# Kernel optimization log

Hardware: AMD Instinct MI355X
Metric: run time of the kernel (lower is better)

Reference implementation:

```python
import jax, jax.numpy as jnp
import numpy as np

B, F_IN, C_NODES, M = 8, 32, 256, 64
C_OUT = 64
ORDER = 2
N_BASES = 3


def setup_inputs() -> dict:
    key = jax.random.key(0)
    ks = jax.random.split(key, 6)
    x = jax.random.normal(ks[0], (B, F_IN, C_NODES, M), dtype=jnp.float32)
    base0 = jax.random.uniform(ks[1], (B, M, C_NODES, C_NODES), dtype=jnp.float32) / C_NODES
    base1 = jax.random.uniform(ks[2], (B, M, C_NODES, C_NODES), dtype=jnp.float32) / C_NODES
    base2 = jax.random.uniform(ks[3], (B, M, C_NODES, C_NODES), dtype=jnp.float32) / C_NODES
    c_cat = (ORDER * N_BASES + 1) * F_IN  # 224
    W = jax.random.normal(ks[4], (C_OUT, c_cat), dtype=jnp.float32) * (1.0 / np.sqrt(c_cat))
    b = jnp.zeros((C_OUT,), dtype=jnp.float32)
    return {"x": x, "base0": base0, "base1": base1, "base2": base2, "W": W, "b": b}


def _nconv(x, A):
    # x: [B, F, n, M], A: [B, M, n, v] -> [B, F, v, M]
    return jnp.einsum('bfnm,bmnv->bfvm', x, A)


def reference(x, base0, base1, base2, W, b):
    out = [x]
    for A in (base0, base1, base2):
        x1 = _nconv(x, A)
        out.append(x1)
        for _ in range(2, ORDER + 1):
            x1 = _nconv(x1, A)
            out.append(x1)
    h = jnp.concatenate(out, axis=1)  # [B, 7F, C, M]
    # 1x1 conv == channel-mixing GEMM
    y = jnp.einsum('of,bfcm->bocm', W, h) + b[None, :, None, None]
    return y
```

## Files before the change

kernel.cpp:

```cpp
#include <hip/hip_runtime.h>

typedef __attribute__((ext_vector_type(8))) short short8;
typedef __attribute__((ext_vector_type(4))) float floatx4;
typedef unsigned short u16;
typedef unsigned int u32;

#define GETC(v, hw) ((hw)==0 ? (v).x : (hw)==1 ? (v).y : (hw)==2 ? (v).z : (v).w)
#define MFMA16(a,b,c) __builtin_amdgcn_mfma_f32_16x16x32_bf16((a),(b),(c),0,0,0)

__device__ __forceinline__ u16 f2bf(float f) {
  u32 u = __builtin_bit_cast(u32, f);
  u += 0x7fffu + ((u >> 16) & 1u);
  return (u16)(u >> 16);
}
__device__ __forceinline__ u32 pk2(float a, float b) {
  return (u32)f2bf(a) | ((u32)f2bf(b) << 16);
}

__global__ __launch_bounds__(256) void tk_f2b(const float* __restrict__ in,
                                              u16* __restrict__ out,
                                              int NI, int NJ) {
  __shared__ float tile[64][65];
  const int tid = threadIdx.x;
  const long long base = (long long)blockIdx.z * NI * NJ;
  const int i0 = blockIdx.x * 64, j0 = blockIdx.y * 64;
#pragma unroll
  for (int p = 0; p < 4; ++p) {
    int i = p * 16 + (tid >> 4);
    int jl = (tid & 15) * 4;
    float4 v = *(const float4*)(in + base + (long long)(i0 + i) * NJ + j0 + jl);
    tile[i][jl + 0] = v.x; tile[i][jl + 1] = v.y;
    tile[i][jl + 2] = v.z; tile[i][jl + 3] = v.w;
  }
  __syncthreads();
#pragma unroll
  for (int p = 0; p < 4; ++p) {
    int j = p * 16 + (tid >> 4);
    int il = (tid & 15) * 4;
    float e0 = tile[il + 0][j], e1 = tile[il + 1][j];
    float e2 = tile[il + 2][j], e3 = tile[il + 3][j];
    uint2 o; o.x = pk2(e0, e1); o.y = pk2(e2, e3);
    *(uint2*)(out + base + (long long)(j0 + j) * NI + i0 + il) = o;
  }
}

__global__ __launch_bounds__(256) void tk_f2f(const float* __restrict__ in,
                                              float* __restrict__ out,
                                              int NI, int NJ) {
  __shared__ float tile[64][65];
  const int tid = threadIdx.x;
  const long long base = (long long)blockIdx.z * NI * NJ;
  const int i0 = blockIdx.x * 64, j0 = blockIdx.y * 64;
#pragma unroll
  for (int p = 0; p < 4; ++p) {
    int i = p * 16 + (tid >> 4);
    int jl = (tid & 15) * 4;
    float4 v = *(const float4*)(in + base + (long long)(i0 + i) * NJ + j0 + jl);
    tile[i][jl + 0] = v.x; tile[i][jl + 1] = v.y;
    tile[i][jl + 2] = v.z; tile[i][jl + 3] = v.w;
  }
  __syncthreads();
#pragma unroll
  for (int p = 0; p < 4; ++p) {
    int j = p * 16 + (tid >> 4);
    int il = (tid & 15) * 4;
    float4 o;
    o.x = tile[il + 0][j]; o.y = tile[il + 1][j];
    o.z = tile[il + 2][j]; o.w = tile[il + 3][j];
    *(float4*)(out + base + (long long)(j0 + j) * NI + i0 + il) = o;
  }
}

__global__ __launch_bounds__(256, 1) void gcn_main(
    const u16* __restrict__ xT, const float* __restrict__ A0,
    const float* __restrict__ A1, const float* __restrict__ A2,
    const float* __restrict__ Wm, const float* __restrict__ bias,
    float* __restrict__ yT) {
  __shared__ __align__(16) unsigned char smem[163840];
  unsigned char* fragA  = smem;
  unsigned char* fragX1 = smem + 131072;
  unsigned char* fragH  = smem + 147456;

  const int tid  = threadIdx.x;
  const int w    = tid >> 6;
  const int lane = tid & 63;
  const int q    = lane >> 4;
  const int s    = lane & 15;
  const int wg   = blockIdx.x;

  const float* Ab0 = A0 + (size_t)wg * 65536;
  const float* Ab1 = A1 + (size_t)wg * 65536;
  const float* Ab2 = A2 + (size_t)wg * 65536;

  short8 xa[2][8];
  const u16* xp = xT + (size_t)wg * 8192;
#pragma unroll
  for (int mr = 0; mr < 2; ++mr)
#pragma unroll
    for (int k = 0; k < 8; ++k)
      xa[mr][k] = *(const short8*)(xp + (16 * mr + s) * 256 + 32 * k + 8 * q);

  const int bn = tid >> 5, bv = tid & 31;
  const int v0 = bv * 8;
  uint4 stg[4][8];
  auto loadStage = [&](const float* Ai) {
#pragma unroll
    for (int p = 0; p < 4; ++p) {
      int n0 = p * 64 + bn * 8;
#pragma unroll
      for (int jj = 0; jj < 8; ++jj) {
        const float* rp = Ai + (size_t)(n0 + jj) * 256 + v0;
        float4 lo = *(const float4*)rp;
        float4 hi = *(const float4*)(rp + 4);
        uint4 r;
        r.x = pk2(lo.x, lo.y); r.y = pk2(lo.z, lo.w);
        r.z = pk2(hi.x, hi.y); r.w = pk2(hi.z, hi.w);
        stg[p][jj] = r;
      }
    }
  };
  auto stageToLds = [&]() {
#pragma unroll
    for (int p = 0; p < 4; ++p) {
      int n0 = p * 64 + bn * 8;
      int kst = n0 >> 5, qst = (n0 >> 3) & 3;
#pragma unroll
      for (int i = 0; i < 8; ++i) {
        int v = v0 + i;
        int tg = v >> 4, sl = v & 15;
        u32 sel = (i & 1) ? 0x07060302u : 0x05040100u;
        const int hw = i >> 1;
        u32 d0 = __builtin_amdgcn_perm(GETC(stg[p][1], hw), GETC(stg[p][0], hw), sel);
        u32 d1 = __builtin_amdgcn_perm(GETC(stg[p][3], hw), GETC(stg[p][2], hw), sel);
        u32 d2 = __builtin_amdgcn_perm(GETC(stg[p][5], hw), GETC(stg[p][4], hw), sel);
        u32 d3 = __builtin_amdgcn_perm(GETC(stg[p][7], hw), GETC(stg[p][6], hw), sel);
        int phys = (qst * 16 + sl) ^ (tg & 7);
        uint4 val; val.x = d0; val.y = d1; val.z = d2; val.w = d3;
        *(uint4*)(fragA + (((kst * 16 + tg) * 64 + phys) << 4)) = val;
      }
    }
  };

  loadStage(Ab0);

#pragma unroll
  for (int mr = 0; mr < 2; ++mr)
#pragma unroll
    for (int kk = 0; kk < 8; ++kk) {
      if ((kk >> 1) != w) continue;
#pragma unroll
      for (int jj = 0; jj < 8; ++jj) {
        int c = 32 * kk + 8 * q + jj;
        int f = 16 * mr + s;
        int off = (((c >> 4) * 64 + (f >> 3) * 16 + (c & 15)) << 4) + 2 * (f & 7);
        *(u16*)(fragH + off) = (u16)xa[mr][kk][jj];
      }
    }

  floatx4 yacc[4][4];
#pragma unroll
  for (int mr = 0; mr < 4; ++mr)
#pragma unroll
    for (int t = 0; t < 4; ++t) yacc[mr][t] = (floatx4){0.f, 0.f, 0.f, 0.f};

  auto finalGemm = [&](int jblk) {
    short8 wf[4], hf[4];
#pragma unroll
    for (int mr = 0; mr < 4; ++mr) {
      const float* wp = Wm + (16 * mr + s) * 224 + 32 * jblk + 8 * q;
      float4 lo = *(const float4*)wp;
      float4 hi = *(const float4*)(wp + 4);
      union { uint4 u; short8 v; } r;
      r.u.x = pk2(lo.x, lo.y); r.u.y = pk2(lo.z, lo.w);
      r.u.z = pk2(hi.x, hi.y); r.u.w = pk2(hi.z, hi.w);
      wf[mr] = r.v;
    }
#pragma unroll
    for (int t = 0; t < 4; ++t)
      hf[t] = *(const short8*)(fragH + (((4 * w + t) * 64 + lane) << 4));
#pragma unroll
    for (int mr = 0; mr < 4; ++mr)
#pragma unroll
      for (int t = 0; t < 4; ++t)
        yacc[mr][t] = MFMA16(wf[mr], hf[t], yacc[mr][t]);
  };
  auto writeH = [&](const floatx4 (&acc)[2][4]) {
#pragma unroll
    for (int mr = 0; mr < 2; ++mr)
#pragma unroll
      for (int t = 0; t < 4; ++t)
#pragma unroll
        for (int r = 0; r < 4; ++r) {
          int F = 16 * mr + 4 * q + r;
          int off = (((4 * w + t) * 64 + (F >> 3) * 16 + s) << 4) + 2 * (F & 7);
          *(u16*)(fragH + off) = f2bf(acc[mr][t][r]);
        }
  };
  auto writeX1 = [&](const floatx4 (&acc)[2][4]) {
#pragma unroll
    for (int mr = 0; mr < 2; ++mr)
#pragma unroll
      for (int t = 0; t < 4; ++t) {
        int Cc = 64 * w + 16 * t + s;
        int kk = Cc >> 5, qq = (Cc >> 3) & 3, jj = Cc & 7;
#pragma unroll
        for (int r = 0; r < 4; ++r) {
          int off = (((mr * 8 + kk) * 64 + qq * 16 + 4 * q + r) << 4) + 2 * jj;
          *(u16*)(fragX1 + off) = f2bf(acc[mr][t][r]);
        }
      }
  };

  __syncthreads();
  finalGemm(0);

#pragma unroll 1
  for (int ib = 0; ib < 3; ++ib) {
    __syncthreads();
    stageToLds();
    if (ib < 2) loadStage(ib == 0 ? Ab1 : Ab2);
    __syncthreads();

    floatx4 h1[2][4];
#pragma unroll
    for (int mr = 0; mr < 2; ++mr)
#pragma unroll
      for (int t = 0; t < 4; ++t) h1[mr][t] = (floatx4){0.f, 0.f, 0.f, 0.f};
#pragma unroll
    for (int k = 0; k < 8; ++k) {
      short8 bf[4];
#pragma unroll
      for (int t = 0; t < 4; ++t) {
        int tg = 4 * w + t;
        bf[t] = *(const short8*)(fragA + (((k * 16 + tg) * 64 + (lane ^ (tg & 7))) << 4));
      }
#pragma unroll
      for (int mr = 0; mr < 2; ++mr)
#pragma unroll
        for (int t = 0; t < 4; ++t)
          h1[mr][t] = MFMA16(xa[mr][k], bf[t], h1[mr][t]);
    }
    writeX1(h1);
    writeH(h1);
    __syncthreads();
    finalGemm(1 + 2 * ib);

    floatx4 h2[2][4];
#pragma unroll
    for (int mr = 0; mr < 2; ++mr)
#pragma unroll
      for (int t = 0; t < 4; ++t) h2[mr][t] = (floatx4){0.f, 0.f, 0.f, 0.f};
#pragma unroll
    for (int k = 0; k < 8; ++k) {
      short8 a0 = *(const short8*)(fragX1 + ((k * 64 + lane) << 4));
      short8 a1 = *(const short8*)(fragX1 + (((8 + k) * 64 + lane) << 4));
      short8 bf[4];
#pragma unroll
      for (int t = 0; t < 4; ++t) {
        int tg = 4 * w + t;
        bf[t] = *(const short8*)(fragA + (((k * 16 + tg) * 64 + (lane ^ (tg & 7))) << 4));
      }
#pragma unroll
      for (int t = 0; t < 4; ++t) {
        h2[0][t] = MFMA16(a0, bf[t], h2[0][t]);
        h2[1][t] = MFMA16(a1, bf[t], h2[1][t]);
      }
    }
    __syncthreads();
    writeH(h2);
    __syncthreads();
    finalGemm(2 + 2 * ib);
  }

  float* yp = yT + (size_t)wg * 16384;
#pragma unroll
  for (int mr = 0; mr < 4; ++mr) {
    float br[4];
#pragma unroll
    for (int r = 0; r < 4; ++r) br[r] = bias[16 * mr + 4 * q + r];
#pragma unroll
    for (int t = 0; t < 4; ++t) {
      int c = 64 * w + 16 * t + s;
#pragma unroll
      for (int r = 0; r < 4; ++r) {
        int o = 16 * mr + 4 * q + r;
        yp[o * 256 + c] = yacc[mr][t][r] + br[r];
      }
    }
  }
}

extern "C" void kernel_launch(void* const* d_in, const int* in_sizes, int n_in,
                              void* d_out, int out_size, void* d_ws, size_t ws_size,
                              hipStream_t stream) {
  const float* x    = (const float*)d_in[0];
  const float* b0   = (const float*)d_in[1];
  const float* b1   = (const float*)d_in[2];
  const float* b2   = (const float*)d_in[3];
  const float* Wm   = (const float*)d_in[4];
  const float* bias = (const float*)d_in[5];
  u16*   xT  = (u16*)d_ws;
  float* yTs = (float*)((char*)d_ws + 8388608);
  float* out = (float*)d_out;

  tk_f2b<<<dim3(128, 1, 8), 256, 0, stream>>>(x, xT, 8192, 64);
  gcn_main<<<dim3(512), 256, 0, stream>>>(xT, b0, b1, b2, Wm, bias, yTs);
  tk_f2f<<<dim3(1, 256, 8), 256, 0, stream>>>(yTs, out, 64, 16384);
}
```

Measured before the change: 443.9 us.

## Stream A tiles via global_load_lds ring buffer, halve LDS for two blocks/CU

Replaces the register-staged full 128KB bf16 copy of each adjacency matrix in LDS with a 3-slot fp32 ring buffer filled by async global_load_lds. Each k-chunk is streamed and converted to bf16 at fragment-read time. The A matrix is re-streamed for both the order-1 and order-2 passes. This cuts LDS to 80KB so two workgroups can share a CU, and it overlaps global loads with MFMA, but the adjacency data is now read from global memory twice and converted repeatedly. It also drops several block barriers, relying on per-wave private ring slices plus vmcnt waits, which risks races around the fragH/fragX1 writes.

```diff
diff --git a/kernel.cpp b/kernel.cpp
--- a/kernel.cpp
+++ b/kernel.cpp
@@ -5,8 +5,26 @@
 typedef unsigned short u16;
 typedef unsigned int u32;
 
-#define GETC(v, hw) ((hw)==0 ? (v).x : (hw)==1 ? (v).y : (hw)==2 ? (v).z : (v).w)
 #define MFMA16(a,b,c) __builtin_amdgcn_mfma_f32_16x16x32_bf16((a),(b),(c),0,0,0)
+
+#define GLD_LDS16(src, dst)                                                    \
+  __builtin_amdgcn_global_load_lds(                                            \
+      (const __attribute__((address_space(1))) u32*)(const u32*)(src),         \
+      (__attribute__((address_space(3))) u32*)(u32*)(dst), 16, 0, 0)
+
+#define WAITVM(N)                                                              \
+  do {                                                                         \
+    asm volatile("s_waitcnt vmcnt(" #N ")" ::: "memory");                      \
+    __builtin_amdgcn_sched_barrier(0);                                         \
+  } while (0)
+
+#define WAITLGKM0() asm volatile("s_waitcnt lgkmcnt(0)" ::: "memory")
+
+__device__ __forceinline__ void bar_lds() {
+  WAITLGKM0();
+  __builtin_amdgcn_s_barrier();
+  asm volatile("" ::: "memory");
+}
 
 __device__ __forceinline__ u16 f2bf(float f) {
   u32 u = __builtin_bit_cast(u32, f);
@@ -71,15 +89,15 @@
   }
 }
 
-__global__ __launch_bounds__(256, 1) void gcn_main(
+__global__ __launch_bounds__(256, 2) void gcn_main(
     const u16* __restrict__ xT, const float* __restrict__ A0,
     const float* __restrict__ A1, const float* __restrict__ A2,
     const float* __restrict__ Wm, const float* __restrict__ bias,
     float* __restrict__ yT) {
-  __shared__ __align__(16) unsigned char smem[163840];
-  unsigned char* fragA  = smem;
-  unsigned char* fragX1 = smem + 131072;
-  unsigned char* fragH  = smem + 147456;
+  __shared__ __align__(16) unsigned char smem[81920];
+  unsigned char* ring   = smem;
+  unsigned char* fragX1 = smem + 49152;
+  unsigned char* fragH  = smem + 65536;
 
   const int tid  = threadIdx.x;
   const int w    = tid >> 6;
@@ -88,9 +106,26 @@
   const int s    = lane & 15;
   const int wg   = blockIdx.x;
 
-  const float* Ab0 = A0 + (size_t)wg * 65536;
-  const float* Ab1 = A1 + (size_t)wg * 65536;
-  const float* Ab2 = A2 + (size_t)wg * 65536;
+  const float* Acur  = A0 + (size_t)wg * 65536;
+  const float* Anxt  = A1 + (size_t)wg * 65536;
+  const float* Alast = A2 + (size_t)wg * 65536;
+
+  const int lrow = (lane >> 4) << 8;
+  const int lc0  = (w << 6) + ((lane & 15) << 2);
+  const int lc1  = lc0 ^ 16;
+  char* wring = (char*)ring + (w << 12);
+
+  auto stage = [&](const float* Ap, int c, int slot) {
+#pragma unroll
+    for (int i = 0; i < 4; ++i) {
+      const float* src = Ap + (c << 12) + (i << 10) + lrow + ((i & 2) ? lc1 : lc0);
+      GLD_LDS16(src, wring + slot * 16384 + (i << 10));
+    }
+  };
+
+  stage(Acur, 0, 0);
+  stage(Acur, 1, 1);
+  stage(Acur, 2, 2);
 
   short8 xa[2][8];
   const u16* xp = xT + (size_t)wg * 8192;
@@ -99,49 +134,6 @@
 #pragma unroll
     for (int k = 0; k < 8; ++k)
       xa[mr][k] = *(const short8*)(xp + (16 * mr + s) * 256 + 32 * k + 8 * q);
-
-  const int bn = tid >> 5, bv = tid & 31;
-  const int v0 = bv * 8;
-  uint4 stg[4][8];
-  auto loadStage = [&](const float* Ai) {
-#pragma unroll
-    for (int p = 0; p < 4; ++p) {
-      int n0 = p * 64 + bn * 8;
-#pragma unroll
-      for (int jj = 0; jj < 8; ++jj) {
-        const float* rp = Ai + (size_t)(n0 + jj) * 256 + v0;
-        float4 lo = *(const float4*)rp;
-        float4 hi = *(const float4*)(rp + 4);
-        uint4 r;
-        r.x = pk2(lo.x, lo.y); r.y = pk2(lo.z, lo.w);
-        r.z = pk2(hi.x, hi.y); r.w = pk2(hi.z, hi.w);
-        stg[p][jj] = r;
-      }
-    }
-  };
-  auto stageToLds = [&]() {
-#pragma unroll
-    for (int p = 0; p < 4; ++p) {
-      int n0 = p * 64 + bn * 8;
-      int kst = n0 >> 5, qst = (n0 >> 3) & 3;
-#pragma unroll
-      for (int i = 0; i < 8; ++i) {
-        int v = v0 + i;
-        int tg = v >> 4, sl = v & 15;
-        u32 sel = (i & 1) ? 0x07060302u : 0x05040100u;
-        const int hw = i >> 1;
-        u32 d0 = __builtin_amdgcn_perm(GETC(stg[p][1], hw), GETC(stg[p][0], hw), sel);
-        u32 d1 = __builtin_amdgcn_perm(GETC(stg[p][3], hw), GETC(stg[p][2], hw), sel);
-        u32 d2 = __builtin_amdgcn_perm(GETC(stg[p][5], hw), GETC(stg[p][4], hw), sel);
-        u32 d3 = __builtin_amdgcn_perm(GETC(stg[p][7], hw), GETC(stg[p][6], hw), sel);
-        int phys = (qst * 16 + sl) ^ (tg & 7);
-        uint4 val; val.x = d0; val.y = d1; val.z = d2; val.w = d3;
-        *(uint4*)(fragA + (((kst * 16 + tg) * 64 + phys) << 4)) = val;
-      }
-    }
-  };
-
-  loadStage(Ab0);
 
 #pragma unroll
   for (int mr = 0; mr < 2; ++mr)
@@ -211,38 +203,55 @@
       }
   };
 
-  __syncthreads();
+  auto fetchB = [&](int sl0, int sl1, short8 (&bf)[4]) {
+    const char* bse = (const char*)ring + ((q >= 2) ? sl1 : sl0) * 16384 +
+                      (w << 12) + ((q & 1) << 11);
+    const int pvx = (q & 1) << 4;
+#pragma unroll
+    for (int t = 0; t < 4; ++t) {
+      const float* fp = (const float*)(bse + ((((t << 4) + s) ^ pvx) << 2));
+      union { uint4 u; short8 v; } r;
+      r.u.x = pk2(fp[0],   fp[64]);
+      r.u.y = pk2(fp[128], fp[192]);
+      r.u.z = pk2(fp[256], fp[320]);
+      r.u.w = pk2(fp[384], fp[448]);
+      bf[t] = r.v;
+    }
+  };
+
   finalGemm(0);
 
 #pragma unroll 1
   for (int ib = 0; ib < 3; ++ib) {
-    __syncthreads();
-    stageToLds();
-    if (ib < 2) loadStage(ib == 0 ? Ab1 : Ab2);
-    __syncthreads();
-
     floatx4 h1[2][4];
 #pragma unroll
     for (int mr = 0; mr < 2; ++mr)
 #pragma unroll
       for (int t = 0; t < 4; ++t) h1[mr][t] = (floatx4){0.f, 0.f, 0.f, 0.f};
 #pragma unroll
-    for (int k = 0; k < 8; ++k) {
+    for (int kk = 0; kk < 8; ++kk) {
+      if (kk < 7) WAITVM(4); else WAITVM(0);
       short8 bf[4];
-#pragma unroll
-      for (int t = 0; t < 4; ++t) {
-        int tg = 4 * w + t;
-        bf[t] = *(const short8*)(fragA + (((k * 16 + tg) * 64 + (lane ^ (tg & 7))) << 4));
-      }
+      fetchB((2 * kk) % 3, (2 * kk + 1) % 3, bf);
 #pragma unroll
       for (int mr = 0; mr < 2; ++mr)
 #pragma unroll
         for (int t = 0; t < 4; ++t)
-          h1[mr][t] = MFMA16(xa[mr][k], bf[t], h1[mr][t]);
-    }
+          h1[mr][t] = MFMA16(xa[mr][kk], bf[t], h1[mr][t]);
+      WAITLGKM0();
+      if (kk < 6) {
+        stage(Acur, 2 * kk + 3, (2 * kk + 3) % 3);
+        stage(Acur, 2 * kk + 4, (2 * kk + 4) % 3);
+      } else if (kk == 6) {
+        stage(Acur, 15, 0);
+      } else {
+        stage(Acur, 0, 0); stage(Acur, 1, 1); stage(Acur, 2, 2);
+      }
+    }
+    bar_lds();
     writeX1(h1);
     writeH(h1);
-    __syncthreads();
+    bar_lds();
     finalGemm(1 + 2 * ib);
 
     floatx4 h2[2][4];
@@ -251,25 +260,31 @@
 #pragma unroll
       for (int t = 0; t < 4; ++t) h2[mr][t] = (floatx4){0.f, 0.f, 0.f, 0.f};
 #pragma unroll
-    for (int k = 0; k < 8; ++k) {
-      short8 a0 = *(const short8*)(fragX1 + ((k * 64 + lane) << 4));
-      short8 a1 = *(const short8*)(fragX1 + (((8 + k) * 64 + lane) << 4));
+    for (int kk = 0; kk < 8; ++kk) {
+      if (kk < 7) WAITVM(4); else WAITVM(0);
       short8 bf[4];
-#pragma unroll
-      for (int t = 0; t < 4; ++t) {
-        int tg = 4 * w + t;
-        bf[t] = *(const short8*)(fragA + (((k * 16 + tg) * 64 + (lane ^ (tg & 7))) << 4));
-      }
+      fetchB((2 * kk) % 3, (2 * kk + 1) % 3, bf);
+      short8 a0 = *(const short8*)(fragX1 + ((kk * 64 + lane) << 4));
+      short8 a1 = *(const short8*)(fragX1 + (((8 + kk) * 64 + lane) << 4));
 #pragma unroll
       for (int t = 0; t < 4; ++t) {
         h2[0][t] = MFMA16(a0, bf[t], h2[0][t]);
         h2[1][t] = MFMA16(a1, bf[t], h2[1][t]);
       }
-    }
-    __syncthreads();
+      WAITLGKM0();
+      if (kk < 6) {
+        stage(Acur, 2 * kk + 3, (2 * kk + 3) % 3);
+        stage(Acur, 2 * kk + 4, (2 * kk + 4) % 3);
+      } else if (kk == 6) {
+        stage(Acur, 15, 0);
+      } else if (ib < 2) {
+        stage(Anxt, 0, 0); stage(Anxt, 1, 1); stage(Anxt, 2, 2);
+      }
+    }
     writeH(h2);
-    __syncthreads();
     finalGemm(2 + 2 * ib);
+
+    Acur = Anxt; Anxt = Alast;
   }
 
   float* yp = yT + (size_t)wg * 16384;
```

New measurement: 481.6 us. +8.5%, slower.
